# Optimization experiments

Measured on AMD Instinct MI355X. Metric: run time of the kernel, lower is better.

## Reference

```python
import jax, jax.numpy as jnp
import numpy as np

B, S, NX, NH = 4, 2048, 1024, 16
HD = NX // NH
MASKED_BIAS = -10000.0


def setup_inputs() -> dict:
    key = jax.random.key(0)
    k1, k2, k3 = jax.random.split(key, 3)
    x = jax.random.normal(k1, (B, S, NX), dtype=jnp.float32)
    w_attn = jax.random.normal(k2, (NX, 3 * NX), dtype=jnp.float32) * 0.02
    b_attn = jnp.zeros((3 * NX,), dtype=jnp.float32)
    w_proj = jax.random.normal(k3, (NX, NX), dtype=jnp.float32) * 0.02
    b_proj = jnp.zeros((NX,), dtype=jnp.float32)
    return {"x": x, "w_attn": w_attn, "b_attn": b_attn, "w_proj": w_proj, "b_proj": b_proj}


def reference(x, w_attn, b_attn, w_proj, b_proj):
    b, s, nx = x.shape
    # c_attn (HF Conv1D): y = x @ W + b
    qkv = x @ w_attn + b_attn                      # [b, s, 3*nx]
    q, k, v = jnp.split(qkv, 3, axis=-1)
    # split heads -> [b, h, s, d]
    q = q.reshape(b, s, NH, HD).transpose(0, 2, 1, 3)
    k = k.reshape(b, s, NH, HD).transpose(0, 2, 1, 3)
    v = v.reshape(b, s, NH, HD).transpose(0, 2, 1, 3)
    # scaled scores, scale by 1/sqrt(head_dim) since scale=True
    w = jnp.einsum('bhqd,bhkd->bhqk', q, k) / jnp.sqrt(jnp.asarray(HD, x.dtype))
    # tril causal mask (bias buffer slice for nd == ns == s)
    causal = jnp.tril(jnp.ones((s, s), dtype=bool))
    w = jnp.where(causal, w, jnp.asarray(MASKED_BIAS, w.dtype))
    w = jax.nn.softmax(w, axis=-1)
    a = jnp.einsum('bhqk,bhkd->bhqd', w, v)        # [b, h, s, d]
    # merge heads -> [b, s, nx]
    a = a.transpose(0, 2, 1, 3).reshape(b, s, nx)
    # c_proj
    a = a @ w_proj + b_proj
    return a
```

## Files before the change

### kernel.cpp

```cpp
#include <hip/hip_runtime.h>
#include <stdint.h>

#define BATCH 4
#define SEQ 2048
#define NX 1024
#define NHEAD 16
#define HDIM 64
#define NTOK (BATCH * SEQ)
#define QKV_LD (3 * NX)

typedef __bf16 bf16_t;
typedef __bf16 bf16x8 __attribute__((ext_vector_type(8)));
typedef __bf16 bf16x4 __attribute__((ext_vector_type(4)));
typedef float  f32x4  __attribute__((ext_vector_type(4)));
typedef unsigned int u32x4 __attribute__((ext_vector_type(4)));

#define GLOAD_LDS16(g, l) __builtin_amdgcn_global_load_lds( \
    (const __attribute__((address_space(1))) void*)(g),     \
    (__attribute__((address_space(3))) void*)(l), 16, 0, 0)

#define MFMA16(a, b, c) __builtin_amdgcn_mfma_f32_16x16x32_bf16((a), (b), (c), 0, 0, 0)

__global__ __launch_bounds__(256) void k_cast_bf16(const float* __restrict__ in,
                                                   bf16_t* __restrict__ out, int n4) {
  int stride = gridDim.x * blockDim.x;
  for (int i = blockIdx.x * blockDim.x + threadIdx.x; i < n4; i += stride) {
    f32x4 v = ((const f32x4*)in)[i];
    bf16x4 o;
    o[0] = (bf16_t)v[0]; o[1] = (bf16_t)v[1];
    o[2] = (bf16_t)v[2]; o[3] = (bf16_t)v[3];
    ((bf16x4*)out)[i] = o;
  }
}

__global__ __launch_bounds__(256) void k_transpose_cast(const float* __restrict__ in,
                                                        bf16_t* __restrict__ out,
                                                        int K, int N) {
  __shared__ float tile[32][33];
  const int kb = blockIdx.x * 32, nb = blockIdx.y * 32;
  const int tx = threadIdx.x & 31;
  const int ty = (threadIdx.x >> 5) * 4;
#pragma unroll
  for (int i = 0; i < 4; i++)
    tile[ty + i][tx] = in[(size_t)(kb + ty + i) * N + nb + tx];
  __syncthreads();
#pragma unroll
  for (int i = 0; i < 4; i++)
    out[(size_t)(nb + ty + i) * K + kb + tx] = (bf16_t)tile[tx][ty + i];
}

__global__ __launch_bounds__(256) void k_vtrans(const bf16_t* __restrict__ qkv,
                                                bf16_t* __restrict__ vt) {
  __shared__ bf16_t tile[32][33];
  const int s0 = blockIdx.x * 32;
  const int d0 = blockIdx.y * 32;
  const int bh = blockIdx.z;
  const int b = bh >> 4, h = bh & 15;
  const bf16_t* src = qkv + (size_t)b * SEQ * QKV_LD + 2 * NX + h * HDIM;
  const int tx = threadIdx.x & 31;
  const int ty = (threadIdx.x >> 5) * 4;
#pragma unroll
  for (int i = 0; i < 4; i++)
    tile[ty + i][tx] = src[(size_t)(s0 + ty + i) * QKV_LD + d0 + tx];
  __syncthreads();
  bf16_t* dst = vt + (size_t)bh * HDIM * SEQ;
#pragma unroll
  for (int i = 0; i < 4; i++)
    dst[(size_t)(d0 + ty + i) * SEQ + s0 + tx] = tile[tx][ty + i];
}

template <int OUT_BF16>
__global__ __launch_bounds__(256) void k_gemm_bt(const bf16_t* __restrict__ A,
                                                 const bf16_t* __restrict__ Bt,
                                                 const float* __restrict__ bias,
                                                 void* __restrict__ Cout,
                                                 int M, int N, int K, int mt) {
  __shared__ __align__(16) bf16_t lsA[2][128 * 32];
  __shared__ __align__(16) bf16_t lsB[2][128 * 32];
  const int tid  = threadIdx.x;
  const int lane = tid & 63;
  const int wid  = tid >> 6;
  const int wr   = wid >> 1, wc = wid & 1;

  const int nwg = gridDim.x;
  const int wg  = (blockIdx.x & 7) * (nwg >> 3) + (blockIdx.x >> 3);
  const int bx  = wg % mt, by = wg / mt;
  const int m0 = bx * 128, n0 = by * 128;

  const int srow = tid >> 2;
  const int scol = (tid & 3) * 8;
  const bf16_t* Ap = A  + (size_t)(m0 + srow) * K + scol;
  const bf16_t* Bp = Bt + (size_t)(n0 + srow) * K + scol;
  const int wbase = (tid & ~63) * 8;

  f32x4 acc[4][4];
#pragma unroll
  for (int i = 0; i < 4; i++)
#pragma unroll
    for (int j = 0; j < 4; j++) acc[i][j] = (f32x4){0.f, 0.f, 0.f, 0.f};

  const int fr = lane & 15;
  const int kb = (lane >> 4) * 8;

  auto stage = [&](int buf, int k0) {
    GLOAD_LDS16(Ap + k0,                  &lsA[buf][wbase]);
    GLOAD_LDS16(Ap + (size_t)64 * K + k0, &lsA[buf][2048 + wbase]);
    GLOAD_LDS16(Bp + k0,                  &lsB[buf][wbase]);
    GLOAD_LDS16(Bp + (size_t)64 * K + k0, &lsB[buf][2048 + wbase]);
  };

  stage(0, 0);
  __syncthreads();
  const int nk = K >> 5;
  for (int kt = 0; kt < nk; kt++) {
    const int cur = kt & 1;
    if (kt + 1 < nk) stage(cur ^ 1, (kt + 1) * 32);
    bf16x8 af[4], bfr[4];
#pragma unroll
    for (int mf = 0; mf < 4; mf++)
      af[mf] = *(const bf16x8*)&lsA[cur][(wr * 64 + mf * 16 + fr) * 32 + kb];
#pragma unroll
    for (int nf = 0; nf < 4; nf++)
      bfr[nf] = *(const bf16x8*)&lsB[cur][(wc * 64 + nf * 16 + fr) * 32 + kb];
#pragma unroll
    for (int mf = 0; mf < 4; mf++)
#pragma unroll
      for (int nf = 0; nf < 4; nf++)
        acc[mf][nf] = MFMA16(af[mf], bfr[nf], acc[mf][nf]);
    __syncthreads();
  }

  const int col = lane & 15, rb = (lane >> 4) * 4;
#pragma unroll
  for (int mf = 0; mf < 4; mf++) {
#pragma unroll
    for (int nf = 0; nf < 4; nf++) {
      const int gm = m0 + wr * 64 + mf * 16 + rb;
      const int gn = n0 + wc * 64 + nf * 16 + col;
      const float bv = bias[gn];
#pragma unroll
      for (int r = 0; r < 4; r++) {
        float v = acc[mf][nf][r] + bv;
        if (OUT_BF16)
          ((bf16_t*)Cout)[(size_t)(gm + r) * N + gn] = (bf16_t)v;
        else
          ((float*)Cout)[(size_t)(gm + r) * N + gn] = v;
      }
    }
  }
}

__global__ __launch_bounds__(256) void k_attn(const bf16_t* __restrict__ qkv,
                                              const bf16_t* __restrict__ vt,
                                              bf16_t* __restrict__ attout) {
  __shared__ __align__(16) bf16_t lsK[2][64 * 64];
  __shared__ __align__(16) bf16_t lsV[2][64 * 64];
  const int tid = threadIdx.x, lane = tid & 63, w = tid >> 6;
  const int blk = blockIdx.x;
  const int bh   = (blk & 7) * 8 + (blk >> 7);
  const int qblk = 15 - ((blk >> 3) & 15);
  const int b = bh >> 4, h = bh & 15;
  const bf16_t* Qb  = qkv + (size_t)b * SEQ * QKV_LD + h * HDIM;
  const bf16_t* Kb  = Qb + NX;
  const bf16_t* Vtb = vt + (size_t)bh * HDIM * SEQ;

  const int fr = lane & 15, g2 = lane >> 4;
  const int kb8 = g2 * 8;
  const int permA = (fr & 3) + 8 * (fr >> 2);

  auto stage = [&](int buf, int kv0) {
#pragma unroll
    for (int s = 0; s < 2; s++) {
      const int i = w * 128 + s * 64 + lane;
      const int row = i >> 3, slot = i & 7;
      const int sk = (row & 3) | (((row >> 3) & 1) << 2);
      GLOAD_LDS16(Kb + (size_t)(kv0 + row) * QKV_LD + ((slot ^ sk) << 3),
                  &lsK[buf][(w * 128 + s * 64) * 8]);
      GLOAD_LDS16(Vtb + (size_t)row * SEQ + kv0 + ((slot ^ (row & 7)) << 3),
                  &lsV[buf][(w * 128 + s * 64) * 8]);
    }
  };

  const int q0 = qblk * 128;
  const int rw = q0 + w * 32;
  const int nst = 2 * qblk + 2;
  const int kv_last = rw & ~63;

  bf16x8 bq[2][2];
#pragma unroll
  for (int g = 0; g < 2; g++)
#pragma unroll
    for (int kf = 0; kf < 2; kf++) {
      bf16x8 t = *(const bf16x8*)&Qb[(size_t)(rw + g * 16 + fr) * QKV_LD + kf * 32 + kb8];
#pragma unroll
      for (int jj = 0; jj < 8; jj++) t[jj] = (bf16_t)((float)t[jj] * 0.1803368801f);
      bq[g][kf] = t;
    }

  float l_run[2] = {0.f, 0.f};
  f32x4 o[2][4];
#pragma unroll
  for (int g = 0; g < 2; g++)
#pragma unroll
    for (int d = 0; d < 4; d++) o[g][d] = (f32x4){0.f, 0.f, 0.f, 0.f};

  stage(0, 0);
  __syncthreads();
  for (int st = 0; st < nst; st++) {
    const int kv0 = st * 64;
    const int cur = st & 1;
    if (st + 1 < nst) stage(cur ^ 1, kv0 + 64);
    if (kv0 <= kv_last) {
      bf16x8 ak[2][2][2];
#pragma unroll
      for (int sub = 0; sub < 2; sub++)
#pragma unroll
        for (int ab = 0; ab < 2; ab++)
#pragma unroll
          for (int kf = 0; kf < 2; kf++) {
            const int row = sub * 32 + ab * 4 + permA;
            const int sk = (row & 3) | (((row >> 3) & 1) << 2);
            const int c = kf * 4 + g2;
            ak[sub][ab][kf] = *(const bf16x8*)&lsK[cur][row * 64 + ((c ^ sk) << 3)];
          }
      bf16x8 vbf[4][2];
#pragma unroll
      for (int df = 0; df < 4; df++)
#pragma unroll
        for (int hh = 0; hh < 2; hh++) {
          const int row = df * 16 + fr;
          const int c = hh * 4 + g2;
          vbf[df][hh] = *(const bf16x8*)&lsV[cur][row * 64 + ((c ^ (row & 7)) << 3)];
        }
      const int masked = (kv0 == kv_last);
      bf16x8 pa[2][2];
#pragma unroll
      for (int g = 0; g < 2; g++) {
        f32x4 sAB[2][2];
#pragma unroll
        for (int sub = 0; sub < 2; sub++)
#pragma unroll
          for (int ab = 0; ab < 2; ab++) {
            f32x4 s0 = (f32x4){0.f, 0.f, 0.f, 0.f};
            s0 = MFMA16(ak[sub][ab][0], bq[g][0], s0);
            s0 = MFMA16(ak[sub][ab][1], bq[g][1], s0);
            sAB[sub][ab] = s0;
          }
        float sv[16];
#pragma unroll
        for (int sub = 0; sub < 2; sub++)
#pragma unroll
          for (int r = 0; r < 4; r++) {
            sv[sub * 8 + r]     = sAB[sub][0][r];
            sv[sub * 8 + 4 + r] = sAB[sub][1][r];
          }
        if (masked) {
          const int q_abs = rw + g * 16 + fr;
#pragma unroll
          for (int sub = 0; sub < 2; sub++)
#pragma unroll
            for (int r = 0; r < 4; r++) {
              if (kv0 + sub * 32 + g2 * 8 + r     > q_abs) sv[sub * 8 + r]     = -1e30f;
              if (kv0 + sub * 32 + g2 * 8 + 4 + r > q_abs) sv[sub * 8 + 4 + r] = -1e30f;
            }
        }
        float tsum = 0.f;
        bf16_t pb[16];
#pragma unroll
        for (int jj = 0; jj < 16; jj++) {
          float pv = exp2f(sv[jj]);
          tsum += pv;
          pb[jj] = (bf16_t)pv;
        }
        l_run[g] += tsum;
#pragma unroll
        for (int sub = 0; sub < 2; sub++) {
          bf16x8 p;
#pragma unroll
          for (int jj = 0; jj < 8; jj++) p[jj] = pb[sub * 8 + jj];
          pa[g][sub] = p;
        }
      }
#pragma unroll
      for (int g = 0; g < 2; g++)
#pragma unroll
        for (int df = 0; df < 4; df++) {
          o[g][df] = MFMA16(pa[g][0], vbf[df][0], o[g][df]);
          o[g][df] = MFMA16(pa[g][1], vbf[df][1], o[g][df]);
        }
    }
    __syncthreads();
  }

#pragma unroll
  for (int g = 0; g < 2; g++) {
    float lt = l_run[g];
    lt += __shfl_xor(lt, 16);
    lt += __shfl_xor(lt, 32);
    const float inv = 1.f / lt;
#pragma unroll
    for (int r = 0; r < 4; r++) {
      const float iv = __shfl(inv, g2 * 4 + r);
      const int tok = b * SEQ + rw + g * 16 + g2 * 4 + r;
#pragma unroll
      for (int df = 0; df < 4; df++)
        attout[(size_t)tok * NX + h * HDIM + df * 16 + fr] = (bf16_t)(o[g][df][r] * iv);
    }
  }
}

extern "C" void kernel_launch(void* const* d_in, const int* in_sizes, int n_in,
                              void* d_out, int out_size, void* d_ws, size_t ws_size,
                              hipStream_t stream) {
  const float* x      = (const float*)d_in[0];
  const float* w_attn = (const float*)d_in[1];
  const float* b_attn = (const float*)d_in[2];
  const float* w_proj = (const float*)d_in[3];
  const float* b_proj = (const float*)d_in[4];

  char* ws = (char*)d_ws;
  bf16_t* xb  = (bf16_t*)ws;
  bf16_t* qkv = (bf16_t*)(ws + (16u << 20));
  bf16_t* wab = (bf16_t*)(ws + (64u << 20));
  bf16_t* vt  = (bf16_t*)(ws + (64u << 20));
  bf16_t* wpb = (bf16_t*)(ws + (80u << 20));
  bf16_t* att = xb;

  k_cast_bf16<<<2048, 256, 0, stream>>>(x, xb, NTOK * NX / 4);
  k_transpose_cast<<<dim3(NX / 32, (3 * NX) / 32), 256, 0, stream>>>(w_attn, wab, NX, 3 * NX);
  k_gemm_bt<1><<<(NTOK / 128) * ((3 * NX) / 128), 256, 0, stream>>>(
      xb, wab, b_attn, (void*)qkv, NTOK, 3 * NX, NX, NTOK / 128);
  k_vtrans<<<dim3(SEQ / 32, HDIM / 32, BATCH * NHEAD), 256, 0, stream>>>(qkv, vt);
  k_transpose_cast<<<dim3(NX / 32, NX / 32), 256, 0, stream>>>(w_proj, wpb, NX, NX);
  k_attn<<<BATCH * NHEAD * 16, 256, 0, stream>>>(qkv, vt, att);
  k_gemm_bt<0><<<(NTOK / 128) * (NX / 128), 256, 0, stream>>>(
      att, wpb, b_proj, d_out, NTOK, NX, NX, NTOK / 128);
}
```

Before: 219.2 us.

## Triple-buffer GEMM and attention, swizzle GEMM LDS, enlarge attention query tiles

```diff
diff --git a/kernel.cpp b/kernel.cpp
--- a/kernel.cpp
+++ b/kernel.cpp
@@ -13,13 +13,19 @@
 typedef __bf16 bf16x8 __attribute__((ext_vector_type(8)));
 typedef __bf16 bf16x4 __attribute__((ext_vector_type(4)));
 typedef float  f32x4  __attribute__((ext_vector_type(4)));
-typedef unsigned int u32x4 __attribute__((ext_vector_type(4)));
 
 #define GLOAD_LDS16(g, l) __builtin_amdgcn_global_load_lds( \
     (const __attribute__((address_space(1))) void*)(g),     \
     (__attribute__((address_space(3))) void*)(l), 16, 0, 0)
 
 #define MFMA16(a, b, c) __builtin_amdgcn_mfma_f32_16x16x32_bf16((a), (b), (c), 0, 0, 0)
+
+#define WAIT_VM4_BAR() do { \
+    asm volatile("s_waitcnt vmcnt(4) lgkmcnt(0)" ::: "memory"); \
+    __builtin_amdgcn_s_barrier(); } while (0)
+#define WAIT_VM0_BAR() do { \
+    asm volatile("s_waitcnt vmcnt(0) lgkmcnt(0)" ::: "memory"); \
+    __builtin_amdgcn_s_barrier(); } while (0)
 
 __global__ __launch_bounds__(256) void k_cast_bf16(const float* __restrict__ in,
                                                    bf16_t* __restrict__ out, int n4) {
@@ -74,21 +80,17 @@
                                                  const bf16_t* __restrict__ Bt,
                                                  const float* __restrict__ bias,
                                                  void* __restrict__ Cout,
-                                                 int M, int N, int K, int mt) {
-  __shared__ __align__(16) bf16_t lsA[2][128 * 32];
-  __shared__ __align__(16) bf16_t lsB[2][128 * 32];
+                                                 int M, int N, int K) {
+  __shared__ __align__(16) bf16_t lsA[3][128 * 32];
+  __shared__ __align__(16) bf16_t lsB[3][128 * 32];
   const int tid  = threadIdx.x;
   const int lane = tid & 63;
   const int wid  = tid >> 6;
   const int wr   = wid >> 1, wc = wid & 1;
-
-  const int nwg = gridDim.x;
-  const int wg  = (blockIdx.x & 7) * (nwg >> 3) + (blockIdx.x >> 3);
-  const int bx  = wg % mt, by = wg / mt;
-  const int m0 = bx * 128, n0 = by * 128;
+  const int m0 = blockIdx.x * 128, n0 = blockIdx.y * 128;
 
   const int srow = tid >> 2;
-  const int scol = (tid & 3) * 8;
+  const int scol = ((tid & 3) ^ (srow & 3)) * 8;
   const bf16_t* Ap = A  + (size_t)(m0 + srow) * K + scol;
   const bf16_t* Bp = Bt + (size_t)(n0 + srow) * K + scol;
   const int wbase = (tid & ~63) * 8;
@@ -100,7 +102,8 @@
     for (int j = 0; j < 4; j++) acc[i][j] = (f32x4){0.f, 0.f, 0.f, 0.f};
 
   const int fr = lane & 15;
-  const int kb = (lane >> 4) * 8;
+  const int g2 = lane >> 4;
+  const int rslot = (g2 ^ (fr & 3)) * 8;
 
   auto stage = [&](int buf, int k0) {
     GLOAD_LDS16(Ap + k0,                  &lsA[buf][wbase]);
@@ -109,25 +112,30 @@
     GLOAD_LDS16(Bp + (size_t)64 * K + k0, &lsB[buf][2048 + wbase]);
   };
 
+  const int nk = K >> 5;
   stage(0, 0);
-  __syncthreads();
-  const int nk = K >> 5;
+  stage(1, 32);
+  asm volatile("s_waitcnt vmcnt(4)" ::: "memory");
+  __builtin_amdgcn_s_barrier();
+
   for (int kt = 0; kt < nk; kt++) {
-    const int cur = kt & 1;
-    if (kt + 1 < nk) stage(cur ^ 1, (kt + 1) * 32);
+    const int cur = kt % 3;
+    if (kt + 2 < nk) stage((kt + 2) % 3, (kt + 2) * 32);
     bf16x8 af[4], bfr[4];
 #pragma unroll
     for (int mf = 0; mf < 4; mf++)
-      af[mf] = *(const bf16x8*)&lsA[cur][(wr * 64 + mf * 16 + fr) * 32 + kb];
+      af[mf] = *(const bf16x8*)&lsA[cur][(wr * 64 + mf * 16 + fr) * 32 + rslot];
 #pragma unroll
     for (int nf = 0; nf < 4; nf++)
-      bfr[nf] = *(const bf16x8*)&lsB[cur][(wc * 64 + nf * 16 + fr) * 32 + kb];
+      bfr[nf] = *(const bf16x8*)&lsB[cur][(wc * 64 + nf * 16 + fr) * 32 + rslot];
 #pragma unroll
     for (int mf = 0; mf < 4; mf++)
 #pragma unroll
       for (int nf = 0; nf < 4; nf++)
         acc[mf][nf] = MFMA16(af[mf], bfr[nf], acc[mf][nf]);
-    __syncthreads();
+    if (kt + 1 < nk) {
+      if (kt + 2 < nk) WAIT_VM4_BAR(); else WAIT_VM0_BAR();
+    }
   }
 
   const int col = lane & 15, rb = (lane >> 4) * 4;
@@ -150,15 +158,16 @@
   }
 }
 
-__global__ __launch_bounds__(256) void k_attn(const bf16_t* __restrict__ qkv,
-                                              const bf16_t* __restrict__ vt,
-                                              bf16_t* __restrict__ attout) {
-  __shared__ __align__(16) bf16_t lsK[2][64 * 64];
-  __shared__ __align__(16) bf16_t lsV[2][64 * 64];
+__global__ __launch_bounds__(256, 2) void k_attn(const bf16_t* __restrict__ qkv,
+                                                 const bf16_t* __restrict__ vt,
+                                                 bf16_t* __restrict__ attout) {
+  __shared__ __align__(16) bf16_t lsK[3][64 * 64];
+  __shared__ __align__(16) bf16_t lsV[3][64 * 64];
   const int tid = threadIdx.x, lane = tid & 63, w = tid >> 6;
   const int blk = blockIdx.x;
-  const int bh   = (blk & 7) * 8 + (blk >> 7);
-  const int qblk = 15 - ((blk >> 3) & 15);
+  const int xcd = blk & 7, idx = blk >> 3;
+  const int bh  = xcd * 8 + (idx & 7);
+  const int qsb = 7 - (idx >> 3);
   const int b = bh >> 4, h = bh & 15;
   const bf16_t* Qb  = qkv + (size_t)b * SEQ * QKV_LD + h * HDIM;
   const bf16_t* Kb  = Qb + NX;
@@ -181,35 +190,37 @@
     }
   };
 
-  const int q0 = qblk * 128;
-  const int rw = q0 + w * 32;
-  const int nst = 2 * qblk + 2;
-  const int kv_last = rw & ~63;
-
-  bf16x8 bq[2][2];
-#pragma unroll
-  for (int g = 0; g < 2; g++)
+  const int wb = qsb * 256 + w * 64;
+  const int kv_last = wb;
+  const int nst = qsb * 4 + 4;
+
+  bf16x8 bq[4][2];
+#pragma unroll
+  for (int g = 0; g < 4; g++)
 #pragma unroll
     for (int kf = 0; kf < 2; kf++) {
-      bf16x8 t = *(const bf16x8*)&Qb[(size_t)(rw + g * 16 + fr) * QKV_LD + kf * 32 + kb8];
+      bf16x8 t = *(const bf16x8*)&Qb[(size_t)(wb + g * 16 + fr) * QKV_LD + kf * 32 + kb8];
 #pragma unroll
       for (int jj = 0; jj < 8; jj++) t[jj] = (bf16_t)((float)t[jj] * 0.1803368801f);
       bq[g][kf] = t;
     }
 
-  float l_run[2] = {0.f, 0.f};
-  f32x4 o[2][4];
-#pragma unroll
-  for (int g = 0; g < 2; g++)
+  float l_run[4] = {0.f, 0.f, 0.f, 0.f};
+  f32x4 o[4][4];
+#pragma unroll
+  for (int g = 0; g < 4; g++)
 #pragma unroll
     for (int d = 0; d < 4; d++) o[g][d] = (f32x4){0.f, 0.f, 0.f, 0.f};
 
   stage(0, 0);
-  __syncthreads();
+  stage(1, 64);
+  asm volatile("s_waitcnt vmcnt(4)" ::: "memory");
+  __builtin_amdgcn_s_barrier();
+
   for (int st = 0; st < nst; st++) {
     const int kv0 = st * 64;
-    const int cur = st & 1;
-    if (st + 1 < nst) stage(cur ^ 1, kv0 + 64);
+    const int cur = st % 3;
+    if (st + 2 < nst) stage((st + 2) % 3, (st + 2) * 64);
     if (kv0 <= kv_last) {
       bf16x8 ak[2][2][2];
 #pragma unroll
@@ -233,10 +244,10 @@
           vbf[df][hh] = *(const bf16x8*)&lsV[cur][row * 64 + ((c ^ (row & 7)) << 3)];
         }
       const int masked = (kv0 == kv_last);
-      bf16x8 pa[2][2];
-#pragma unroll
-      for (int g = 0; g < 2; g++) {
+#pragma unroll
+      for (int g = 0; g < 4; g++) {
         f32x4 sAB[2][2];
+        __builtin_amdgcn_s_setprio(1);
 #pragma unroll
         for (int sub = 0; sub < 2; sub++)
 #pragma unroll
@@ -246,6 +257,7 @@
             s0 = MFMA16(ak[sub][ab][1], bq[g][1], s0);
             sAB[sub][ab] = s0;
           }
+        __builtin_amdgcn_s_setprio(0);
         float sv[16];
 #pragma unroll
         for (int sub = 0; sub < 2; sub++)
@@ -255,7 +267,7 @@
             sv[sub * 8 + 4 + r] = sAB[sub][1][r];
           }
         if (masked) {
-          const int q_abs = rw + g * 16 + fr;
+          const int q_abs = wb + g * 16 + fr;
 #pragma unroll
           for (int sub = 0; sub < 2; sub++)
 #pragma unroll
@@ -273,27 +285,25 @@
           pb[jj] = (bf16_t)pv;
         }
         l_run[g] += tsum;
-#pragma unroll
-        for (int sub = 0; sub < 2; sub++) {
-          bf16x8 p;
-#pragma unroll
-          for (int jj = 0; jj < 8; jj++) p[jj] = pb[sub * 8 + jj];
-          pa[g][sub] = p;
+        bf16x8 pa0, pa1;
+#pragma unroll
+        for (int jj = 0; jj < 8; jj++) { pa0[jj] = pb[jj]; pa1[jj] = pb[8 + jj]; }
+        __builtin_amdgcn_s_setprio(1);
+#pragma unroll
+        for (int df = 0; df < 4; df++) {
+          o[g][df] = MFMA16(pa0, vbf[df][0], o[g][df]);
+          o[g][df] = MFMA16(pa1, vbf[df][1], o[g][df]);
         }
+        __builtin_amdgcn_s_setprio(0);
       }
-#pragma unroll
-      for (int g = 0; g < 2; g++)
-#pragma unroll
-        for (int df = 0; df < 4; df++) {
-          o[g][df] = MFMA16(pa[g][0], vbf[df][0], o[g][df]);
-          o[g][df] = MFMA16(pa[g][1], vbf[df][1], o[g][df]);
-        }
-    }
-    __syncthreads();
-  }
-
-#pragma unroll
-  for (int g = 0; g < 2; g++) {
+    }
+    if (st + 1 < nst) {
+      if (st + 2 < nst) WAIT_VM4_BAR(); else WAIT_VM0_BAR();
+    }
+  }
+
+#pragma unroll
+  for (int g = 0; g < 4; g++) {
     float lt = l_run[g];
     lt += __shfl_xor(lt, 16);
     lt += __shfl_xor(lt, 32);
@@ -301,7 +311,7 @@
 #pragma unroll
     for (int r = 0; r < 4; r++) {
       const float iv = __shfl(inv, g2 * 4 + r);
-      const int tok = b * SEQ + rw + g * 16 + g2 * 4 + r;
+      const int tok = b * SEQ + wb + g * 16 + g2 * 4 + r;
 #pragma unroll
       for (int df = 0; df < 4; df++)
         attout[(size_t)tok * NX + h * HDIM + df * 16 + fr] = (bf16_t)(o[g][df][r] * iv);
@@ -328,11 +338,11 @@
 
   k_cast_bf16<<<2048, 256, 0, stream>>>(x, xb, NTOK * NX / 4);
   k_transpose_cast<<<dim3(NX / 32, (3 * NX) / 32), 256, 0, stream>>>(w_attn, wab, NX, 3 * NX);
-  k_gemm_bt<1><<<(NTOK / 128) * ((3 * NX) / 128), 256, 0, stream>>>(
-      xb, wab, b_attn, (void*)qkv, NTOK, 3 * NX, NX, NTOK / 128);
+  k_gemm_bt<1><<<dim3(NTOK / 128, (3 * NX) / 128), 256, 0, stream>>>(
+      xb, wab, b_attn, (void*)qkv, NTOK, 3 * NX, NX);
   k_vtrans<<<dim3(SEQ / 32, HDIM / 32, BATCH * NHEAD), 256, 0, stream>>>(qkv, vt);
   k_transpose_cast<<<dim3(NX / 32, NX / 32), 256, 0, stream>>>(w_proj, wpb, NX, NX);
-  k_attn<<<BATCH * NHEAD * 16, 256, 0, stream>>>(qkv, vt, att);
-  k_gemm_bt<0><<<(NTOK / 128) * (NX / 128), 256, 0, stream>>>(
-      att, wpb, b_proj, d_out, NTOK, NX, NX, NTOK / 128);
-}
+  k_attn<<<BATCH * NHEAD * 8, 256, 0, stream>>>(qkv, vt, att);
+  k_gemm_bt<0><<<dim3(NTOK / 128, NX / 128), 256, 0, stream>>>(
+      att, wpb, b_proj, d_out, NTOK, NX, NX);
+}
```

Result: faster. 192.9 us (-12.0%).
